# Kernel optimization log

Measured on AMD Instinct MI355X. Metric: run time of the kernel, lower is better.

## Reference

```python
import jax, jax.numpy as jnp
import numpy as np

V_DIM = 2048
Q_DIM = 1024
B = 64
K = 36


def setup_inputs() -> dict:
    key = jax.random.key(0)
    ks = jax.random.split(key, 6)
    s1 = 1.0 / np.sqrt(2 * V_DIM + Q_DIM)
    s2 = 1.0 / np.sqrt(V_DIM)
    s3 = 1.0 / np.sqrt(Q_DIM)
    return {
        "v": jax.random.normal(ks[0], (B, K, V_DIM), dtype=jnp.float32),
        "q": jax.random.normal(ks[1], (B, Q_DIM), dtype=jnp.float32),
        "W1": jax.random.normal(ks[2], (V_DIM, 2 * V_DIM + Q_DIM), dtype=jnp.float32) * s1,
        "b1": jnp.zeros((V_DIM,), dtype=jnp.float32),
        "W2": jax.random.normal(ks[3], (V_DIM, V_DIM), dtype=jnp.float32) * s2,
        "b2": jnp.zeros((V_DIM,), dtype=jnp.float32),
        "W3": jax.random.normal(ks[4], (Q_DIM, Q_DIM), dtype=jnp.float32) * s3,
        "b3": jnp.zeros((Q_DIM,), dtype=jnp.float32),
    }


def reference(v, q, W1, b1, W2, b2, W3, b3):
    # FCNet = (weight-normed) Linear + ReLU; dropout disabled (eval / p=0).
    vd = W2.shape[0]
    # q embedding: [B, q_dim]
    q_emb = jax.nn.relu(q @ W3.T + b3)
    # Decompose linear1(concat(v_i, v_j, q_emb)) into three matmuls.
    Wa = W1[:, :vd]            # acts on v_i
    Wb = W1[:, vd:2 * vd]      # acts on v_j
    Wc = W1[:, 2 * vd:]        # acts on q_emb
    a = jnp.einsum('bkd,vd->bkv', v, Wa)          # [B, K, v_dim]
    bpart = jnp.einsum('bkd,vd->bkv', v, Wb)      # [B, K, v_dim]
    c = jnp.einsum('bq,vq->bv', q_emb, Wc) + b1   # [B, v_dim]
    # Pairwise ReLU then sum over j: [B, K_i, K_j, v_dim] -> [B, K, v_dim]
    pair = jax.nn.relu(a[:, :, None, :] + bpart[:, None, :, :] + c[:, None, None, :])
    x = jnp.sum(pair, axis=2)
    # linear2 + ReLU
    return jax.nn.relu(jnp.einsum('bkv,wv->bkw', x, W2) + b2)
```

## Files before the change

### kernel.cpp

```cpp
#include <hip/hip_runtime.h>

#define V_DIMC 2048
#define Q_DIMC 1024
#define BATCH  64
#define KC     36
#define MROWS  (BATCH * KC)
#define W1LD   (2 * V_DIMC + Q_DIMC)

typedef __bf16 bf16_t;
typedef __attribute__((ext_vector_type(8))) __bf16 bf16x8;
typedef __attribute__((ext_vector_type(4))) __bf16 bf16x4;
typedef __attribute__((ext_vector_type(4))) float f32x4;

__device__ __forceinline__ void gload16(const bf16_t* g, bf16_t* l) {
    __builtin_amdgcn_global_load_lds(
        (const __attribute__((address_space(1))) unsigned int*)(g),
        (__attribute__((address_space(3))) unsigned int*)(l), 16, 0, 0);
}

#define MFMAI(a, b, c) __builtin_amdgcn_mfma_f32_16x16x32_bf16(a, b, c, 0, 0, 0)
#define BARX() __builtin_amdgcn_s_barrier()
#define VMC(n)  asm volatile("s_waitcnt vmcnt(" #n ")" ::: "memory")

__global__ __launch_bounds__(256) void conv_all(const float* __restrict__ v,
                                                const float* __restrict__ q,
                                                const float* __restrict__ W1,
                                                const float* __restrict__ W2,
                                                const float* __restrict__ W3,
                                                bf16_t* __restrict__ Wab,
                                                bf16_t* __restrict__ W2b,
                                                bf16_t* __restrict__ vb,
                                                bf16_t* __restrict__ W3b,
                                                bf16_t* __restrict__ Wcb,
                                                bf16_t* __restrict__ qb) {
    const int t = blockIdx.x * 256 + threadIdx.x;
    const float* src;
    bf16_t* dst;
    if (t < 2097152) {
        size_t idx = (size_t)t * 4;
        int row = (int)(idx >> 11), col = (int)(idx & 2047);
        src = (row < 2048) ? W1 + (size_t)row * W1LD + col
                           : W1 + (size_t)(row - 2048) * W1LD + V_DIMC + col;
        dst = Wab + idx;
    } else if (t < 3145728) {
        size_t idx = (size_t)(t - 2097152) * 4;
        src = W2 + idx; dst = W2b + idx;
    } else if (t < 4325376) {
        size_t idx = (size_t)(t - 3145728) * 4;
        src = v + idx; dst = vb + idx;
    } else if (t < 4587520) {
        size_t idx = (size_t)(t - 4325376) * 4;
        src = W3 + idx; dst = W3b + idx;
    } else if (t < 5111808) {
        size_t idx = (size_t)(t - 4587520) * 4;
        int row = (int)(idx >> 10), col = (int)(idx & 1023);
        src = W1 + (size_t)row * W1LD + 2 * V_DIMC + col;
        dst = Wcb + idx;
    } else {
        size_t idx = (size_t)(t - 5111808) * 4;
        src = q + idx; dst = qb + idx;
    }
    float4 f = *reinterpret_cast<const float4*>(src);
    bf16x4 o;
    o[0] = (bf16_t)f.x; o[1] = (bf16_t)f.y; o[2] = (bf16_t)f.z; o[3] = (bf16_t)f.w;
    *reinterpret_cast<bf16x4*>(dst) = o;
}

template <int MODE>
__global__ __launch_bounds__(512) void qgemm(const bf16_t* __restrict__ A,
                                             const bf16_t* __restrict__ B,
                                             void* __restrict__ out,
                                             const float* __restrict__ bias) {
    constexpr int K = 1024;
    constexpr int NDIM = (MODE == 0) ? Q_DIMC : V_DIMC;
    __shared__ float red[8][4096];
    const int tid = threadIdx.x;
    const int w = tid >> 6, l = tid & 63;
    const int n0 = blockIdx.x * 64;
    const int fr = l & 15, lq = l >> 4;
    const bf16_t* Ab = A + (size_t)(w * 128) + lq * 8;
    const bf16_t* Bb = B + (size_t)n0 * K + (size_t)(w * 128) + lq * 8;

    f32x4 acc[4][4] = {};
#pragma unroll
    for (int ks = 0; ks < 4; ++ks) {
        bf16x8 aF[4], bF[4];
#pragma unroll
        for (int mi = 0; mi < 4; ++mi)
            aF[mi] = *(const bf16x8*)(Ab + (size_t)(mi * 16 + fr) * K + ks * 32);
#pragma unroll
        for (int ni = 0; ni < 4; ++ni)
            bF[ni] = *(const bf16x8*)(Bb + (size_t)(ni * 16 + fr) * K + ks * 32);
#pragma unroll
        for (int mi = 0; mi < 4; ++mi)
#pragma unroll
            for (int ni = 0; ni < 4; ++ni)
                acc[mi][ni] = MFMAI(aF[mi], bF[ni], acc[mi][ni]);
    }

    const int rb = lq * 4;
#pragma unroll
    for (int mi = 0; mi < 4; ++mi)
#pragma unroll
        for (int ni = 0; ni < 4; ++ni)
#pragma unroll
            for (int j = 0; j < 4; ++j)
                red[w][(mi * 16 + rb + j) * 64 + ni * 16 + fr] = acc[mi][ni][j];
    __syncthreads();

    const int row = tid >> 3, cb = (tid & 7) * 8;
    float s[8] = {};
#pragma unroll
    for (int ww = 0; ww < 8; ++ww) {
        f32x4 v0 = *(const f32x4*)&red[ww][row * 64 + cb];
        f32x4 v1 = *(const f32x4*)&red[ww][row * 64 + cb + 4];
#pragma unroll
        for (int j = 0; j < 4; ++j) { s[j] += v0[j]; s[4 + j] += v1[j]; }
    }
    if (MODE == 0) {
        bf16x8 o;
#pragma unroll
        for (int j = 0; j < 8; ++j)
            o[j] = (bf16_t)fmaxf(s[j] + bias[n0 + cb + j], 0.f);
        *reinterpret_cast<bf16x8*>((bf16_t*)out + (size_t)row * NDIM + n0 + cb) = o;
    } else {
        float4 r0, r1;
        float* rr[2] = {&r0.x, &r1.x};
#pragma unroll
        for (int h = 0; h < 2; ++h)
#pragma unroll
            for (int j = 0; j < 4; ++j)
                rr[h][j] = s[h * 4 + j] + bias[n0 + cb + h * 4 + j];
        float* op = (float*)out + (size_t)row * NDIM + n0 + cb;
        *reinterpret_cast<float4*>(op) = r0;
        *reinterpret_cast<float4*>(op + 4) = r1;
    }
}

template <int MODE, int MF>
__global__ __launch_bounds__(512) void gemm1b(const bf16_t* __restrict__ A,
                                              const bf16_t* __restrict__ Bm,
                                              bf16_t* __restrict__ out0,
                                              bf16_t* __restrict__ out1,
                                              bf16_t* __restrict__ out2) {
    constexpr int K = 2048;
    constexpr int MH = MF / 2;
    const int z = (MODE == 2) ? (int)blockIdx.z : 0;
    const int NT = (MODE == 2) ? ((z == 2) ? 10 : 11) : 32;
    const int kb = (MODE == 2) ? z * 704 : 0;
    __shared__ bf16_t ldsA[2][MF * 2048];
    __shared__ bf16_t ldsB[2][2][8192];
    const int tid = threadIdx.x;
    const int w = tid >> 6, l = tid & 63;
    const int wm = w >> 2, wn = w & 3;

    int bx, by;
    if (MODE == 0) {
        const int flat = (int)blockIdx.y * 16 + (int)blockIdx.x;
        const int xcd = flat & 7, idx = flat >> 3;
        bx = (xcd & 3) * 4 + (idx & 3);
        by = (xcd >> 2) * 6 + (idx >> 2);
    } else {
        bx = (int)blockIdx.x; by = (int)blockIdx.y;
    }
    const int m0 = by * (MF * 32);
    const int n0 = bx * 256;
    const size_t sK = (size_t)K;

    const int arow = tid >> 3;
    const bf16_t* gA = A + (size_t)(m0 + arow) * sK + kb
                         + (size_t)(((tid & 7) ^ (arow & 7)) << 3);
    const int brow = tid >> 2;
    const bf16_t* gB = Bm + (size_t)(n0 + brow) * sK + kb
                          + (size_t)(((tid & 3) ^ ((tid >> 3) & 3)) << 3);
    const int stW = w * 512;

    auto STGA = [&](int T) {
#pragma unroll
        for (int p = 0; p < MH; ++p)
            gload16(gA + (size_t)(p * 64) * sK + (size_t)T * 64,
                    &ldsA[T & 1][p * 4096 + stW]);
    };
    auto STGB = [&](int ks, int T) {
        const bf16_t* g_ = gB + (size_t)T * 64 + ks * 32;
        gload16(g_, &ldsB[T & 1][ks][stW]);
        gload16(g_ + (size_t)128 * sK, &ldsB[T & 1][ks][4096 + stW]);
    };

    const int fr = l & 15, lq = l >> 4;
    const int sw0 = (lq ^ (fr & 7)) << 4;
    const int sw1 = ((4 | lq) ^ (fr & 7)) << 4;
    const int bsw = (lq ^ ((fr >> 1) & 3)) << 4;
    const int aro = fr * 128;
    const int bro = (wn * 64 + fr) * 64 + bsw;

    f32x4 acc[MF][4] = {};

    STGA(0);
    STGB(0, 0);
    STGB(1, 0);
    VMC(0);
    BARX();

    for (int T = 0; T < NT; ++T) {
        const char* pa  = (const char*)&ldsA[T & 1][0] + wm * (MF * 2048);
        const char* pb0 = (const char*)&ldsB[T & 1][0][0];
        const char* pb1 = (const char*)&ldsB[T & 1][1][0];
        bf16x8 aF[MF], bF[4];

        if (T + 1 < NT) {
            STGA(T + 1);
            STGB(0, T + 1);
            STGB(1, T + 1);
        }

#pragma unroll
        for (int mi = 0; mi < MF; ++mi)
            aF[mi] = *(const bf16x8*)(pa + mi * 2048 + aro + sw0);
#pragma unroll
        for (int ni = 0; ni < 4; ++ni)
            bF[ni] = *(const bf16x8*)(pb0 + bro + ni * 1024);
        __builtin_amdgcn_s_setprio(1);
#pragma unroll
        for (int mi = 0; mi < MF; ++mi)
#pragma unroll
            for (int ni = 0; ni < 4; ++ni)
                acc[mi][ni] = MFMAI(aF[mi], bF[ni], acc[mi][ni]);
        __builtin_amdgcn_s_setprio(0);

#pragma unroll
        for (int mi = 0; mi < MF; ++mi)
            aF[mi] = *(const bf16x8*)(pa + mi * 2048 + aro + sw1);
#pragma unroll
        for (int ni = 0; ni < 4; ++ni)
            bF[ni] = *(const bf16x8*)(pb1 + bro + ni * 1024);
        __builtin_amdgcn_s_setprio(1);
#pragma unroll
        for (int mi = 0; mi < MF; ++mi)
#pragma unroll
            for (int ni = 0; ni < 4; ++ni)
                acc[mi][ni] = MFMAI(aF[mi], bF[ni], acc[mi][ni]);
        __builtin_amdgcn_s_setprio(0);

        VMC(0);
        BARX();
    }

    bf16_t* o;
    int gn0;
    if (MODE == 0) {
        if (n0 < V_DIMC) { o = out0; gn0 = n0; }
        else             { o = out1; gn0 = n0 - V_DIMC; }
    } else {
        o = (z == 0) ? out0 : (z == 1) ? out1 : out2;
        gn0 = n0;
    }
    const int rb = lq * 4;
#pragma unroll
    for (int mi = 0; mi < MF; ++mi)
#pragma unroll
        for (int ni = 0; ni < 4; ++ni) {
            const size_t gm = (size_t)(m0 + wm * (MF * 16) + mi * 16 + rb);
            const int gn = gn0 + wn * 64 + ni * 16 + fr;
#pragma unroll
            for (int r = 0; r < 4; ++r)
                o[(gm + r) * V_DIMC + gn] = (bf16_t)acc[mi][ni][r];
        }
}

__global__ __launch_bounds__(256) void reduce_out(const bf16_t* __restrict__ p0,
                                                  const bf16_t* __restrict__ p1,
                                                  const bf16_t* __restrict__ p2,
                                                  const float* __restrict__ b2,
                                                  float* __restrict__ out) {
    const size_t t = (size_t)blockIdx.x * 256 + threadIdx.x;
    const size_t idx = t * 8;
    bf16x8 a = *reinterpret_cast<const bf16x8*>(p0 + idx);
    bf16x8 b = *reinterpret_cast<const bf16x8*>(p1 + idx);
    bf16x8 c = *reinterpret_cast<const bf16x8*>(p2 + idx);
    const int col = (int)(idx & (V_DIMC - 1));
    float4 r0, r1;
    float* rr[2] = {&r0.x, &r1.x};
#pragma unroll
    for (int h = 0; h < 2; ++h)
#pragma unroll
        for (int j = 0; j < 4; ++j)
            rr[h][j] = fmaxf((float)a[h * 4 + j] + (float)b[h * 4 + j] +
                             (float)c[h * 4 + j] + b2[col + h * 4 + j], 0.f);
    *reinterpret_cast<float4*>(out + idx) = r0;
    *reinterpret_cast<float4*>(out + idx + 4) = r1;
}

__global__ __launch_bounds__(256) void pair_kernel(const bf16_t* __restrict__ A,
                                                   const bf16_t* __restrict__ Bp,
                                                   const float* __restrict__ cbuf,
                                                   bf16_t* __restrict__ X) {
    const int v = blockIdx.x * 256 + threadIdx.x;
    const int b = blockIdx.y;
    const float cc = cbuf[b * V_DIMC + v];
    const bf16_t* Ab = A + (size_t)b * KC * V_DIMC + v;
    const bf16_t* Bb = Bp + (size_t)b * KC * V_DIMC + v;
    float av[KC], bv[KC];
#pragma unroll
    for (int k = 0; k < KC; ++k) {
        av[k] = (float)Ab[(size_t)k * V_DIMC] + cc;
        bv[k] = (float)Bb[(size_t)k * V_DIMC];
    }
    bf16_t* Xb = X + (size_t)b * KC * V_DIMC + v;
#pragma unroll
    for (int k = 0; k < KC; ++k) {
        float s = 0.f;
#pragma unroll
        for (int j = 0; j < KC; ++j) s += fmaxf(av[k] + bv[j], 0.f);
        Xb[(size_t)k * V_DIMC] = (bf16_t)s;
    }
}

extern "C" void kernel_launch(void* const* d_in, const int* in_sizes, int n_in,
                              void* d_out, int out_size, void* d_ws, size_t ws_size,
                              hipStream_t stream) {
    const float* v  = (const float*)d_in[0];
    const float* q  = (const float*)d_in[1];
    const float* W1 = (const float*)d_in[2];
    const float* b1 = (const float*)d_in[3];
    const float* W2 = (const float*)d_in[4];
    const float* b2 = (const float*)d_in[5];
    const float* W3 = (const float*)d_in[6];
    const float* b3 = (const float*)d_in[7];
    float* out = (float*)d_out;

    char* wsb = (char*)d_ws;
    bf16_t* Wab_b = (bf16_t*)wsb;
    bf16_t* W2b   = (bf16_t*)(wsb + 16777216ull);
    bf16_t* vb    = (bf16_t*)(wsb + 25165824ull);
    bf16_t* Abf   = (bf16_t*)(wsb + 34603008ull);
    bf16_t* W3b   = (bf16_t*)(wsb + 34603008ull);
    bf16_t* Wcb   = (bf16_t*)(wsb + 34603008ull + 2097152);
    bf16_t* qb    = (bf16_t*)(wsb + 34603008ull + 6291456);
    bf16_t* Bbf   = (bf16_t*)(wsb + 44040192ull);
    bf16_t* qemb  = (bf16_t*)(wsb + 53477376ull);
    float*  cbuf  = (float*) (wsb + 53608448ull);
    bf16_t* Xb    = Wab_b;

    conv_all<<<dim3(20032), 256, 0, stream>>>(v, q, W1, W2, W3, Wab_b, W2b, vb, W3b, Wcb, qb);
    qgemm<0><<<dim3(Q_DIMC / 64), 512, 0, stream>>>(qb, W3b, qemb, b3);
    qgemm<1><<<dim3(V_DIMC / 64), 512, 0, stream>>>(qemb, Wcb, cbuf, b1);

    gemm1b<0, 6><<<dim3(4096 / 256, MROWS / 192), 512, 0, stream>>>(vb, Wab_b, Abf, Bbf, nullptr);
    pair_kernel<<<dim3(V_DIMC / 256, BATCH), 256, 0, stream>>>(Abf, Bbf, cbuf, Xb);
    gemm1b<2, 8><<<dim3(V_DIMC / 256, MROWS / 256, 3), 512, 0, stream>>>(Xb, W2b, Abf, Bbf, vb);
    reduce_out<<<dim3((MROWS * V_DIMC / 8) / 256), 256, 0, stream>>>(Abf, Bbf, vb, b2, out);
}
```

Measured before the change: 152.3 us.

## Replace large GEMM tiles with 128x128 tiles and 2-way split-K

Replaces the 512-thread GEMM with large M tiles (192/256 x 256) by a 256-thread kernel using 128x128 tiles for both the v-projection and the linear2 GEMM. The second GEMM switches from a 3-way to a 2-way split-K, so the final reduction reads one fewer partial buffer. The LDS reads are now issued before the next-stage prefetch, with extra barriers and lgkmcnt waits around the MFMA blocks. This gives more blocks and better CU occupancy on a GPU with many CUs, at the cost of less operand reuse per tile, more global traffic and more barriers.

```diff
diff --git a/kernel.cpp b/kernel.cpp
--- a/kernel.cpp
+++ b/kernel.cpp
@@ -20,6 +20,7 @@
 
 #define MFMAI(a, b, c) __builtin_amdgcn_mfma_f32_16x16x32_bf16(a, b, c, 0, 0, 0)
 #define BARX() __builtin_amdgcn_s_barrier()
+#define LGKM0() asm volatile("s_waitcnt lgkmcnt(0)" ::: "memory")
 #define VMC(n)  asm volatile("s_waitcnt vmcnt(" #n ")" ::: "memory")
 
 __global__ __launch_bounds__(256) void conv_all(const float* __restrict__ v,
@@ -137,111 +138,100 @@
     }
 }
 
-template <int MODE, int MF>
-__global__ __launch_bounds__(512) void gemm1b(const bf16_t* __restrict__ A,
+template <int MODE>
+__global__ __launch_bounds__(256) void gemm2b(const bf16_t* __restrict__ A,
                                               const bf16_t* __restrict__ Bm,
                                               bf16_t* __restrict__ out0,
-                                              bf16_t* __restrict__ out1,
-                                              bf16_t* __restrict__ out2) {
+                                              bf16_t* __restrict__ out1) {
     constexpr int K = 2048;
-    constexpr int MH = MF / 2;
     const int z = (MODE == 2) ? (int)blockIdx.z : 0;
-    const int NT = (MODE == 2) ? ((z == 2) ? 10 : 11) : 32;
-    const int kb = (MODE == 2) ? z * 704 : 0;
-    __shared__ bf16_t ldsA[2][MF * 2048];
-    __shared__ bf16_t ldsB[2][2][8192];
+    const int NT = (MODE == 2) ? 16 : 32;
+    const int kb = (MODE == 2) ? z * 1024 : 0;
+    __shared__ bf16_t ldsA[2][8192];
+    __shared__ bf16_t ldsB[2][8192];
     const int tid = threadIdx.x;
     const int w = tid >> 6, l = tid & 63;
-    const int wm = w >> 2, wn = w & 3;
+    const int wm = w >> 1, wnn = w & 1;
 
     int bx, by;
     if (MODE == 0) {
-        const int flat = (int)blockIdx.y * 16 + (int)blockIdx.x;
+        const int flat = (int)blockIdx.y * 32 + (int)blockIdx.x;
         const int xcd = flat & 7, idx = flat >> 3;
-        bx = (xcd & 3) * 4 + (idx & 3);
-        by = (xcd >> 2) * 6 + (idx >> 2);
+        bx = xcd * 4 + (idx & 3);
+        by = idx >> 2;
     } else {
         bx = (int)blockIdx.x; by = (int)blockIdx.y;
     }
-    const int m0 = by * (MF * 32);
-    const int n0 = bx * 256;
+    const int m0 = by * 128;
+    const int n0 = bx * 128;
     const size_t sK = (size_t)K;
 
-    const int arow = tid >> 3;
-    const bf16_t* gA = A + (size_t)(m0 + arow) * sK + kb
-                         + (size_t)(((tid & 7) ^ (arow & 7)) << 3);
-    const int brow = tid >> 2;
-    const bf16_t* gB = Bm + (size_t)(n0 + brow) * sK + kb
-                          + (size_t)(((tid & 3) ^ ((tid >> 3) & 3)) << 3);
+    const int srow = tid >> 3;
+    const int sunit = ((tid & 7) ^ (srow & 7)) << 3;
+    const bf16_t* gA = A  + (size_t)(m0 + srow) * sK + kb + sunit;
+    const bf16_t* gB = Bm + (size_t)(n0 + srow) * sK + kb + sunit;
     const int stW = w * 512;
 
     auto STGA = [&](int T) {
 #pragma unroll
-        for (int p = 0; p < MH; ++p)
-            gload16(gA + (size_t)(p * 64) * sK + (size_t)T * 64,
-                    &ldsA[T & 1][p * 4096 + stW]);
+        for (int p = 0; p < 4; ++p)
+            gload16(gA + (size_t)(p * 32) * sK + (size_t)T * 64,
+                    &ldsA[T & 1][p * 2048 + stW]);
     };
-    auto STGB = [&](int ks, int T) {
-        const bf16_t* g_ = gB + (size_t)T * 64 + ks * 32;
-        gload16(g_, &ldsB[T & 1][ks][stW]);
-        gload16(g_ + (size_t)128 * sK, &ldsB[T & 1][ks][4096 + stW]);
+    auto STGB = [&](int T) {
+#pragma unroll
+        for (int p = 0; p < 4; ++p)
+            gload16(gB + (size_t)(p * 32) * sK + (size_t)T * 64,
+                    &ldsB[T & 1][p * 2048 + stW]);
     };
 
     const int fr = l & 15, lq = l >> 4;
     const int sw0 = (lq ^ (fr & 7)) << 4;
     const int sw1 = ((4 | lq) ^ (fr & 7)) << 4;
-    const int bsw = (lq ^ ((fr >> 1) & 3)) << 4;
     const int aro = fr * 128;
-    const int bro = (wn * 64 + fr) * 64 + bsw;
-
-    f32x4 acc[MF][4] = {};
-
-    STGA(0);
-    STGB(0, 0);
-    STGB(1, 0);
+
+    f32x4 acc[4][4] = {};
+
+    STGA(0); STGB(0);
     VMC(0);
     BARX();
 
     for (int T = 0; T < NT; ++T) {
-        const char* pa  = (const char*)&ldsA[T & 1][0] + wm * (MF * 2048);
-        const char* pb0 = (const char*)&ldsB[T & 1][0][0];
-        const char* pb1 = (const char*)&ldsB[T & 1][1][0];
-        bf16x8 aF[MF], bF[4];
-
-        if (T + 1 < NT) {
-            STGA(T + 1);
-            STGB(0, T + 1);
-            STGB(1, T + 1);
-        }
-
-#pragma unroll
-        for (int mi = 0; mi < MF; ++mi)
+        const char* pa = (const char*)&ldsA[T & 1][0] + wm * 8192;
+        const char* pb = (const char*)&ldsB[T & 1][0] + wnn * 8192;
+        bf16x8 aF[4], bF[4];
+
+#pragma unroll
+        for (int mi = 0; mi < 4; ++mi)
             aF[mi] = *(const bf16x8*)(pa + mi * 2048 + aro + sw0);
 #pragma unroll
         for (int ni = 0; ni < 4; ++ni)
-            bF[ni] = *(const bf16x8*)(pb0 + bro + ni * 1024);
+            bF[ni] = *(const bf16x8*)(pb + ni * 2048 + aro + sw0);
+        if (T + 1 < NT) { STGA(T + 1); STGB(T + 1); }
+        BARX(); LGKM0();
         __builtin_amdgcn_s_setprio(1);
 #pragma unroll
-        for (int mi = 0; mi < MF; ++mi)
+        for (int mi = 0; mi < 4; ++mi)
 #pragma unroll
             for (int ni = 0; ni < 4; ++ni)
                 acc[mi][ni] = MFMAI(aF[mi], bF[ni], acc[mi][ni]);
         __builtin_amdgcn_s_setprio(0);
-
-#pragma unroll
-        for (int mi = 0; mi < MF; ++mi)
+        BARX();
+
+#pragma unroll
+        for (int mi = 0; mi < 4; ++mi)
             aF[mi] = *(const bf16x8*)(pa + mi * 2048 + aro + sw1);
 #pragma unroll
         for (int ni = 0; ni < 4; ++ni)
-            bF[ni] = *(const bf16x8*)(pb1 + bro + ni * 1024);
+            bF[ni] = *(const bf16x8*)(pb + ni * 2048 + aro + sw1);
+        BARX(); LGKM0();
         __builtin_amdgcn_s_setprio(1);
 #pragma unroll
-        for (int mi = 0; mi < MF; ++mi)
+        for (int mi = 0; mi < 4; ++mi)
 #pragma unroll
             for (int ni = 0; ni < 4; ++ni)
                 acc[mi][ni] = MFMAI(aF[mi], bF[ni], acc[mi][ni]);
         __builtin_amdgcn_s_setprio(0);
-
         VMC(0);
         BARX();
     }
@@ -252,16 +242,16 @@
         if (n0 < V_DIMC) { o = out0; gn0 = n0; }
         else             { o = out1; gn0 = n0 - V_DIMC; }
     } else {
-        o = (z == 0) ? out0 : (z == 1) ? out1 : out2;
+        o = z ? out1 : out0;
         gn0 = n0;
     }
     const int rb = lq * 4;
 #pragma unroll
-    for (int mi = 0; mi < MF; ++mi)
+    for (int mi = 0; mi < 4; ++mi)
 #pragma unroll
         for (int ni = 0; ni < 4; ++ni) {
-            const size_t gm = (size_t)(m0 + wm * (MF * 16) + mi * 16 + rb);
-            const int gn = gn0 + wn * 64 + ni * 16 + fr;
+            const size_t gm = (size_t)(m0 + wm * 64 + mi * 16 + rb);
+            const int gn = gn0 + wnn * 64 + ni * 16 + fr;
 #pragma unroll
             for (int r = 0; r < 4; ++r)
                 o[(gm + r) * V_DIMC + gn] = (bf16_t)acc[mi][ni][r];
@@ -270,14 +260,12 @@
 
 __global__ __launch_bounds__(256) void reduce_out(const bf16_t* __restrict__ p0,
                                                   const bf16_t* __restrict__ p1,
-                                                  const bf16_t* __restrict__ p2,
                                                   const float* __restrict__ b2,
                                                   float* __restrict__ out) {
     const size_t t = (size_t)blockIdx.x * 256 + threadIdx.x;
     const size_t idx = t * 8;
     bf16x8 a = *reinterpret_cast<const bf16x8*>(p0 + idx);
     bf16x8 b = *reinterpret_cast<const bf16x8*>(p1 + idx);
-    bf16x8 c = *reinterpret_cast<const bf16x8*>(p2 + idx);
     const int col = (int)(idx & (V_DIMC - 1));
     float4 r0, r1;
     float* rr[2] = {&r0.x, &r1.x};
@@ -286,7 +274,7 @@
 #pragma unroll
         for (int j = 0; j < 4; ++j)
             rr[h][j] = fmaxf((float)a[h * 4 + j] + (float)b[h * 4 + j] +
-                             (float)c[h * 4 + j] + b2[col + h * 4 + j], 0.f);
+                             b2[col + h * 4 + j], 0.f);
     *reinterpret_cast<float4*>(out + idx) = r0;
     *reinterpret_cast<float4*>(out + idx + 4) = r1;
 }
@@ -346,8 +334,8 @@
     qgemm<0><<<dim3(Q_DIMC / 64), 512, 0, stream>>>(qb, W3b, qemb, b3);
     qgemm<1><<<dim3(V_DIMC / 64), 512, 0, stream>>>(qemb, Wcb, cbuf, b1);
 
-    gemm1b<0, 6><<<dim3(4096 / 256, MROWS / 192), 512, 0, stream>>>(vb, Wab_b, Abf, Bbf, nullptr);
+    gemm2b<0><<<dim3(32, MROWS / 128), 256, 0, stream>>>(vb, Wab_b, Abf, Bbf);
     pair_kernel<<<dim3(V_DIMC / 256, BATCH), 256, 0, stream>>>(Abf, Bbf, cbuf, Xb);
-    gemm1b<2, 8><<<dim3(V_DIMC / 256, MROWS / 256, 3), 512, 0, stream>>>(Xb, W2b, Abf, Bbf, vb);
-    reduce_out<<<dim3((MROWS * V_DIMC / 8) / 256), 256, 0, stream>>>(Abf, Bbf, vb, b2, out);
-}
+    gemm2b<2><<<dim3(V_DIMC / 128, MROWS / 128, 2), 256, 0, stream>>>(Xb, W2b, Abf, Bbf);
+    reduce_out<<<dim3((MROWS * V_DIMC / 8) / 256), 256, 0, stream>>>(Abf, Bbf, b2, out);
+}
```

Result: slower. 163.7 us (+7.5%).
